# Kernel tuning notes

Hardware: AMD Instinct MI355X
Metric: run time of the kernel (lower is better)

## Reference

```python
import jax, jax.numpy as jnp
import numpy as np

NUM_CAPSULE = 16
DIM_CAPSULE = 16
NUM_ROUTING = 3
EPS = 1e-7  # K.epsilon()


def squash(v, axis=-1):
    s2 = jnp.sum(jnp.square(v), axis=axis, keepdims=True) + EPS
    scale = s2 / ((1.0 + s2) * jnp.sqrt(s2))
    return scale * v


def setup_inputs() -> dict:
    key = jax.random.key(0)
    k1, k2 = jax.random.split(key)
    B, N, IC, ID = 64, 128, 32, 8
    x = jax.random.normal(k1, (B, N, IC, ID), dtype=jnp.float32)
    # glorot_uniform for W: [IC, ID, NUM_CAPSULE*DIM_CAPSULE]
    fan_in, fan_out = ID, NUM_CAPSULE * DIM_CAPSULE
    limit = np.sqrt(6.0 / (fan_in + fan_out))
    W = jax.random.uniform(k2, (IC, ID, NUM_CAPSULE * DIM_CAPSULE), dtype=jnp.float32,
                           minval=-limit, maxval=limit)
    return {"x": x, "W": W}


def reference(x, W):
    B, N, IC, ID = x.shape
    NC, DC = NUM_CAPSULE, DIM_CAPSULE
    u = x.reshape(-1, IC, ID)  # [BN, IC, ID]
    # prediction vectors: [BN, IC, NC*DC] -> [BN, NC, IC, DC]
    u_hat = jnp.einsum('bij,ijk->bik', u, W).reshape(-1, IC, NC, DC).transpose(0, 2, 1, 3)
    u_hat_stopped = jax.lax.stop_gradient(u_hat)
    b = jnp.zeros((u_hat.shape[0], NC, IC), dtype=x.dtype)
    outputs = None
    for i in range(NUM_ROUTING):
        c = jax.nn.softmax(b, axis=1)  # softmax over num_capsule axis (dim=1 in source)
        hat = u_hat if i == NUM_ROUTING - 1 else u_hat_stopped
        outputs = squash(jnp.einsum('bci,bcid->bcd', c, hat))  # [BN, NC, DC]
        if i < NUM_ROUTING - 1:
            b = b + jnp.einsum('bcd,bcid->bci', outputs, u_hat_stopped)
    return outputs.reshape(B, N, NC, DC)
```

## Files before the change

### kernel.cpp

```cpp
#include <hip/hip_runtime.h>
#include <hip/hip_bf16.h>


#define S 2

typedef float    v2f __attribute__((ext_vector_type(2)));
typedef _Float16 v2h __attribute__((ext_vector_type(2)));

template <int CTRL>
__device__ __forceinline__ float dppf(float x) {
  return __builtin_bit_cast(float,
      __builtin_amdgcn_update_dpp(0, __builtin_bit_cast(int, x), CTRL, 0xF, 0xF, true));
}
template <int CTRL>
__device__ __forceinline__ v2f dpp2(v2f v) {
  v2f r;
  r.x = dppf<CTRL>(v.x);
  r.y = dppf<CTRL>(v.y);
  return r;
}
__device__ __forceinline__ float swz4(float x) {
  return __builtin_bit_cast(float,
      __builtin_amdgcn_ds_swizzle(__builtin_bit_cast(int, x), 0x101F));
}
__device__ __forceinline__ v2f swz4_2(v2f v) {
  v2f r;
  r.x = swz4(v.x);
  r.y = swz4(v.y);
  return r;
}

#if __has_builtin(__builtin_amdgcn_fdot2)
__device__ __forceinline__ float dot2(v2h a, v2h b, float c) {
  return __builtin_amdgcn_fdot2(a, b, c, false);
}
#else
__device__ __forceinline__ float dot2(v2h a, v2h b, float c) {
  return fmaf((float)a.x, (float)b.x, fmaf((float)a.y, (float)b.y, c));
}
#endif

__global__ __launch_bounds__(256) void wt_kernel(const float* __restrict__ W,
                                                 _Float16* __restrict__ Wth) {
  int o       = blockIdx.x * 256 + threadIdx.x;
  int ic_slot = o >> 11;
  int k       = (o >> 3) & 255;
  int id      = o & 7;
  int ic_src  = (ic_slot & 16) | ((ic_slot ^ k) & 15);
  Wth[o] = (_Float16)W[(ic_src * 8 + id) * 256 + k];
}

__global__ __launch_bounds__(256) void xh_kernel(const float* __restrict__ x,
                                                 _Float16* __restrict__ xh) {
  int tid = blockIdx.x * 256 + threadIdx.x;
  const float4* xp = (const float4*)x + tid * 2;
  float4 f0 = xp[0], f1 = xp[1];
  v2h h0 = {(_Float16)f0.x, (_Float16)f0.y};
  v2h h1 = {(_Float16)f0.z, (_Float16)f0.w};
  v2h h2 = {(_Float16)f1.x, (_Float16)f1.y};
  v2h h3 = {(_Float16)f1.z, (_Float16)f1.w};
  uint4 o;
  o.x = __builtin_bit_cast(unsigned, h0);
  o.y = __builtin_bit_cast(unsigned, h1);
  o.z = __builtin_bit_cast(unsigned, h2);
  o.w = __builtin_bit_cast(unsigned, h3);
  ((uint4*)xh)[tid] = o;
}

__device__ __forceinline__ v2f squash2(v2f o) {
  v2f s2 = o * o;
  s2 += dpp2<0xB1>(s2);
  s2 += dpp2<0x4E>(s2);
  s2 += dpp2<0x141>(s2);
  s2 += dpp2<0x140>(s2);
  s2 += (v2f){1e-7f, 1e-7f};
  v2f sc;
  sc.x = s2.x * __builtin_amdgcn_rsqf(s2.x) * __builtin_amdgcn_rcpf(1.f + s2.x);
  sc.y = s2.y * __builtin_amdgcn_rsqf(s2.y) * __builtin_amdgcn_rcpf(1.f + s2.y);
  return o * sc;
}

template <bool ASSIGN>
__device__ __forceinline__ void b_update2(v2f v, const v2f* uhx, int dc,
                                          float* bp0, float* bp1) {
#pragma unroll
  for (int icb = 0; icb < 32; icb += 16) {
    v2f y[16];
#pragma unroll
    for (int j = 0; j < 16; ++j) y[j] = v * uhx[icb + j];
#pragma unroll
    for (int j = 0; j < 8; ++j) y[j] += dpp2<0x128>(y[j + 8]);
#pragma unroll
    for (int j = 0; j < 4; ++j) y[j] += swz4_2(y[j + 4]);
#pragma unroll
    for (int j = 0; j < 2; ++j) y[j] += dpp2<0x4E>(y[j + 2]);
    y[0] += dpp2<0xB1>(y[1]);
    if (ASSIGN) { bp0[icb + dc] = y[0].x;  bp1[icb + dc] = y[0].y; }
    else        { bp0[icb + dc] += y[0].x; bp1[icb + dc] += y[0].y; }
  }
}

__global__ __launch_bounds__(256, 3) void caps_kernel(const _Float16* __restrict__ xh,
                                                      const uint4* __restrict__ Wt4,
                                                      float* __restrict__ out) {
  const int t  = threadIdx.x;
  const int nc = t >> 4;
  const int dc = t & 15;
  const int s0 = blockIdx.x * S;

  __shared__ float b_lds[S][16][33];
  __shared__ float c_lds[16][66];

  v2f uhx[32];
  v2f o2 = (v2f){0.f, 0.f};

  const v2h* xp0 = (const v2h*)(xh + (s0 + 0) * 256);
  const v2h* xp1 = (const v2h*)(xh + (s0 + 1) * 256);
#pragma unroll
  for (int ic = 0; ic < 32; ++ic) {
    uint4 wv = Wt4[ic * 256 + t];
    v2h w0 = __builtin_bit_cast(v2h, wv.x);
    v2h w1 = __builtin_bit_cast(v2h, wv.y);
    v2h w2 = __builtin_bit_cast(v2h, wv.z);
    v2h w3 = __builtin_bit_cast(v2h, wv.w);
    const int icx0 = (ic & 16) | ((ic ^ dc) & 15);
    float a0 = dot2(xp0[icx0 * 4 + 3], w3,
               dot2(xp0[icx0 * 4 + 2], w2,
               dot2(xp0[icx0 * 4 + 1], w1,
               dot2(xp0[icx0 * 4 + 0], w0, 0.f))));
    float a1 = dot2(xp1[icx0 * 4 + 3], w3,
               dot2(xp1[icx0 * 4 + 2], w2,
               dot2(xp1[icx0 * 4 + 1], w1,
               dot2(xp1[icx0 * 4 + 0], w0, 0.f))));
    v2f u = (v2f){a0, a1};
    uhx[ic] = u;
    o2 += u;
  }

  {
    v2f v = squash2(o2 * (v2f){0.0625f, 0.0625f});
    b_update2<true>(v, uhx, dc, &b_lds[0][nc][0], &b_lds[1][nc][0]);
  }
  __syncthreads();

#pragma unroll
  for (int r = 1; r < 3; ++r) {
    {
      const int ss  = t >> 7;
      const int icc = (t >> 2) & 31;
      const int q   = t & 3;
      float e0 = __expf(b_lds[ss][4 * q + 0][icc]);
      float e1 = __expf(b_lds[ss][4 * q + 1][icc]);
      float e2 = __expf(b_lds[ss][4 * q + 2][icc]);
      float e3 = __expf(b_lds[ss][4 * q + 3][icc]);
      float ps = (e0 + e1) + (e2 + e3);
      ps += dppf<0xB1>(ps);
      ps += dppf<0x4E>(ps);
      float inv = __builtin_amdgcn_rcpf(ps);
      c_lds[4 * q + 0][2 * icc + ss] = e0 * inv;
      c_lds[4 * q + 1][2 * icc + ss] = e1 * inv;
      c_lds[4 * q + 2][2 * icc + ss] = e2 * inv;
      c_lds[4 * q + 3][2 * icc + ss] = e3 * inv;
    }
    __syncthreads();

    const float2* cpair = (const float2*)&c_lds[nc][0];
    v2f o = (v2f){0.f, 0.f};
#pragma unroll
    for (int j = 0; j < 16; ++j) {
      const int m = j ^ dc;
      float2 cA = cpair[m];
      float2 cB = cpair[m + 16];
      o = __builtin_elementwise_fma((v2f){cA.x, cA.y}, uhx[j], o);
      o = __builtin_elementwise_fma((v2f){cB.x, cB.y}, uhx[16 + j], o);
    }
    v2f v = squash2(o);
    if (r == 2) {
      out[(s0 + 0) * 256 + t] = v.x;
      out[(s0 + 1) * 256 + t] = v.y;
    } else {
      b_update2<false>(v, uhx, dc, &b_lds[0][nc][0], &b_lds[1][nc][0]);
      __syncthreads();
    }
  }
}

extern "C" void kernel_launch(void* const* d_in, const int* in_sizes, int n_in,
                              void* d_out, int out_size, void* d_ws, size_t ws_size,
                              hipStream_t stream) {
  const float* x = (const float*)d_in[0];
  const float* W = (const float*)d_in[1];
  _Float16* Wth = (_Float16*)d_ws;
  _Float16* xh  = (_Float16*)d_ws + 65536;

  wt_kernel<<<256, 256, 0, stream>>>(W, Wth);
  xh_kernel<<<1024, 256, 0, stream>>>(x, xh);
  caps_kernel<<<8192 / S, 256, 0, stream>>>(xh, (const uint4*)Wth, (float*)d_out);
}
```

Baseline: 111.8 us.

## Merge prep kernels, stage x in LDS, replace swizzle with DPP row-xor

The two preprocessing kernels become one launch, removing one kernel launch and its gap. The caps kernel now copies each block's fp16 x slice into shared memory once and reads it as 16-byte LDS vectors instead of scattered global loads. The ds_swizzle xor-4 step in the b-update reduction is replaced by two DPP row-shift moves with bank masks, and the paired DPP ops are split per component. These add a block barrier and LDS traffic in exchange for fewer global loads and launches.

```diff
diff --git a/kernel.cpp b/kernel.cpp
--- a/kernel.cpp
+++ b/kernel.cpp
@@ -19,15 +19,15 @@
   r.y = dppf<CTRL>(v.y);
   return r;
 }
-__device__ __forceinline__ float swz4(float x) {
+template <int CTRL, int BANK>
+__device__ __forceinline__ float dpp_old(float old, float x) {
   return __builtin_bit_cast(float,
-      __builtin_amdgcn_ds_swizzle(__builtin_bit_cast(int, x), 0x101F));
-}
-__device__ __forceinline__ v2f swz4_2(v2f v) {
-  v2f r;
-  r.x = swz4(v.x);
-  r.y = swz4(v.y);
-  return r;
+      __builtin_amdgcn_update_dpp(__builtin_bit_cast(int, old),
+                                  __builtin_bit_cast(int, x), CTRL, 0xF, BANK, false));
+}
+__device__ __forceinline__ float xor4t(float s) {
+  float ya = dpp_old<0x104, 0x5>(0.0f, s);
+  return dpp_old<0x114, 0xA>(ya, s);
 }
 
 #if __has_builtin(__builtin_amdgcn_fdot2)
@@ -40,39 +40,41 @@
 }
 #endif
 
-__global__ __launch_bounds__(256) void wt_kernel(const float* __restrict__ W,
-                                                 _Float16* __restrict__ Wth) {
-  int o       = blockIdx.x * 256 + threadIdx.x;
-  int ic_slot = o >> 11;
-  int k       = (o >> 3) & 255;
-  int id      = o & 7;
-  int ic_src  = (ic_slot & 16) | ((ic_slot ^ k) & 15);
-  Wth[o] = (_Float16)W[(ic_src * 8 + id) * 256 + k];
-}
-
-__global__ __launch_bounds__(256) void xh_kernel(const float* __restrict__ x,
-                                                 _Float16* __restrict__ xh) {
-  int tid = blockIdx.x * 256 + threadIdx.x;
-  const float4* xp = (const float4*)x + tid * 2;
-  float4 f0 = xp[0], f1 = xp[1];
-  v2h h0 = {(_Float16)f0.x, (_Float16)f0.y};
-  v2h h1 = {(_Float16)f0.z, (_Float16)f0.w};
-  v2h h2 = {(_Float16)f1.x, (_Float16)f1.y};
-  v2h h3 = {(_Float16)f1.z, (_Float16)f1.w};
-  uint4 o;
-  o.x = __builtin_bit_cast(unsigned, h0);
-  o.y = __builtin_bit_cast(unsigned, h1);
-  o.z = __builtin_bit_cast(unsigned, h2);
-  o.w = __builtin_bit_cast(unsigned, h3);
-  ((uint4*)xh)[tid] = o;
+__global__ __launch_bounds__(256) void prep_kernel(const float* __restrict__ W,
+                                                   const float* __restrict__ x,
+                                                   _Float16* __restrict__ Wth,
+                                                   _Float16* __restrict__ xh) {
+  int bid = blockIdx.x;
+  if (bid < 256) {
+    int o       = bid * 256 + threadIdx.x;
+    int ic_slot = o >> 11;
+    int k       = (o >> 3) & 255;
+    int id      = o & 7;
+    int ic_src  = (ic_slot & 16) | ((ic_slot ^ k) & 15);
+    Wth[o] = (_Float16)W[(ic_src * 8 + id) * 256 + k];
+  } else {
+    int tid = (bid - 256) * 256 + threadIdx.x;
+    const float4* xp = (const float4*)x + tid * 2;
+    float4 f0 = xp[0], f1 = xp[1];
+    v2h h0 = {(_Float16)f0.x, (_Float16)f0.y};
+    v2h h1 = {(_Float16)f0.z, (_Float16)f0.w};
+    v2h h2 = {(_Float16)f1.x, (_Float16)f1.y};
+    v2h h3 = {(_Float16)f1.z, (_Float16)f1.w};
+    uint4 o;
+    o.x = __builtin_bit_cast(unsigned, h0);
+    o.y = __builtin_bit_cast(unsigned, h1);
+    o.z = __builtin_bit_cast(unsigned, h2);
+    o.w = __builtin_bit_cast(unsigned, h3);
+    ((uint4*)xh)[tid] = o;
+  }
 }
 
 __device__ __forceinline__ v2f squash2(v2f o) {
   v2f s2 = o * o;
-  s2 += dpp2<0xB1>(s2);
-  s2 += dpp2<0x4E>(s2);
-  s2 += dpp2<0x141>(s2);
-  s2 += dpp2<0x140>(s2);
+  s2.x += dppf<0xB1>(s2.x);   s2.y += dppf<0xB1>(s2.y);
+  s2.x += dppf<0x4E>(s2.x);   s2.y += dppf<0x4E>(s2.y);
+  s2.x += dppf<0x141>(s2.x);  s2.y += dppf<0x141>(s2.y);
+  s2.x += dppf<0x140>(s2.x);  s2.y += dppf<0x140>(s2.y);
   s2 += (v2f){1e-7f, 1e-7f};
   v2f sc;
   sc.x = s2.x * __builtin_amdgcn_rsqf(s2.x) * __builtin_amdgcn_rcpf(1.f + s2.x);
@@ -89,18 +91,28 @@
 #pragma unroll
     for (int j = 0; j < 16; ++j) y[j] = v * uhx[icb + j];
 #pragma unroll
-    for (int j = 0; j < 8; ++j) y[j] += dpp2<0x128>(y[j + 8]);
-#pragma unroll
-    for (int j = 0; j < 4; ++j) y[j] += swz4_2(y[j + 4]);
-#pragma unroll
-    for (int j = 0; j < 2; ++j) y[j] += dpp2<0x4E>(y[j + 2]);
-    y[0] += dpp2<0xB1>(y[1]);
+    for (int j = 0; j < 8; ++j) {
+      y[j].x += dppf<0x128>(y[j + 8].x);
+      y[j].y += dppf<0x128>(y[j + 8].y);
+    }
+#pragma unroll
+    for (int j = 0; j < 4; ++j) {
+      y[j].x += xor4t(y[j + 4].x);
+      y[j].y += xor4t(y[j + 4].y);
+    }
+#pragma unroll
+    for (int j = 0; j < 2; ++j) {
+      y[j].x += dppf<0x4E>(y[j + 2].x);
+      y[j].y += dppf<0x4E>(y[j + 2].y);
+    }
+    y[0].x += dppf<0xB1>(y[1].x);
+    y[0].y += dppf<0xB1>(y[1].y);
     if (ASSIGN) { bp0[icb + dc] = y[0].x;  bp1[icb + dc] = y[0].y; }
     else        { bp0[icb + dc] += y[0].x; bp1[icb + dc] += y[0].y; }
   }
 }
 
-__global__ __launch_bounds__(256, 3) void caps_kernel(const _Float16* __restrict__ xh,
+__global__ __launch_bounds__(256, 3) void caps_kernel(const unsigned* __restrict__ xh32,
                                                       const uint4* __restrict__ Wt4,
                                                       float* __restrict__ out) {
   const int t  = threadIdx.x;
@@ -110,12 +122,14 @@
 
   __shared__ float b_lds[S][16][33];
   __shared__ float c_lds[16][66];
+  __shared__ __align__(16) _Float16 xh_lds[2 * 256];
+
+  ((unsigned*)xh_lds)[t] = xh32[s0 * 128 + t];
+  __syncthreads();
 
   v2f uhx[32];
   v2f o2 = (v2f){0.f, 0.f};
 
-  const v2h* xp0 = (const v2h*)(xh + (s0 + 0) * 256);
-  const v2h* xp1 = (const v2h*)(xh + (s0 + 1) * 256);
 #pragma unroll
   for (int ic = 0; ic < 32; ++ic) {
     uint4 wv = Wt4[ic * 256 + t];
@@ -124,14 +138,16 @@
     v2h w2 = __builtin_bit_cast(v2h, wv.z);
     v2h w3 = __builtin_bit_cast(v2h, wv.w);
     const int icx0 = (ic & 16) | ((ic ^ dc) & 15);
-    float a0 = dot2(xp0[icx0 * 4 + 3], w3,
-               dot2(xp0[icx0 * 4 + 2], w2,
-               dot2(xp0[icx0 * 4 + 1], w1,
-               dot2(xp0[icx0 * 4 + 0], w0, 0.f))));
-    float a1 = dot2(xp1[icx0 * 4 + 3], w3,
-               dot2(xp1[icx0 * 4 + 2], w2,
-               dot2(xp1[icx0 * 4 + 1], w1,
-               dot2(xp1[icx0 * 4 + 0], w0, 0.f))));
+    uint4 xv0 = *(const uint4*)(xh_lds + icx0 * 8);
+    uint4 xv1 = *(const uint4*)(xh_lds + 256 + icx0 * 8);
+    float a0 = dot2(__builtin_bit_cast(v2h, xv0.w), w3,
+               dot2(__builtin_bit_cast(v2h, xv0.z), w2,
+               dot2(__builtin_bit_cast(v2h, xv0.y), w1,
+               dot2(__builtin_bit_cast(v2h, xv0.x), w0, 0.f))));
+    float a1 = dot2(__builtin_bit_cast(v2h, xv1.w), w3,
+               dot2(__builtin_bit_cast(v2h, xv1.z), w2,
+               dot2(__builtin_bit_cast(v2h, xv1.y), w1,
+               dot2(__builtin_bit_cast(v2h, xv1.x), w0, 0.f))));
     v2f u = (v2f){a0, a1};
     uhx[ic] = u;
     o2 += u;
@@ -193,7 +209,7 @@
   _Float16* Wth = (_Float16*)d_ws;
   _Float16* xh  = (_Float16*)d_ws + 65536;
 
-  wt_kernel<<<256, 256, 0, stream>>>(W, Wth);
-  xh_kernel<<<1024, 256, 0, stream>>>(x, xh);
-  caps_kernel<<<8192 / S, 256, 0, stream>>>(xh, (const uint4*)Wth, (float*)d_out);
-}
+  prep_kernel<<<1280, 256, 0, stream>>>(W, x, Wth, xh);
+  caps_kernel<<<8192 / S, 256, 0, stream>>>((const unsigned*)xh, (const uint4*)Wth,
+                                            (float*)d_out);
+}
```

After: 97.25 us. 13.0% less time.
